# Kernel tuning notes

Measured on AMD Instinct MI355X. Metric: run time of the kernel, lower is better.

The kernel has to match this reference:

```python
import jax, jax.numpy as jnp
import numpy as np

T = 524288
D = 256
N = 8192

def setup_inputs() -> dict:
    key = jax.random.key(0)
    k1, k2, k3 = jax.random.split(key, 3)
    embedding = jax.random.normal(k1, (T, D), dtype=jnp.float32)
    W = jax.random.normal(k2, (D, D), dtype=jnp.float32) * (1.0 / np.sqrt(D))
    obj_to_img = jnp.sort(jax.random.randint(k3, (T,), 0, N))
    return {"embedding": embedding, "W": W, "obj_to_img": obj_to_img, "num_segments": N}

def reference(embedding, W, obj_to_img, num_segments):
    # Per-segment mean of embedding @ W  -> global context [N, D]
    proj = embedding @ W  # [T, D]
    seg_sum = jax.ops.segment_sum(proj, obj_to_img, num_segments=num_segments)  # [N, D]
    counts = jax.ops.segment_sum(jnp.ones((embedding.shape[0],), embedding.dtype),
                                 obj_to_img, num_segments=num_segments)  # [N]
    safe_counts = jnp.maximum(counts, 1.0)
    transformed_global = jnp.tanh(seg_sum / safe_counts[:, None])  # [N, D]
    # sigmoid(emb . tg[segment]) per token
    scores = jax.nn.sigmoid(jnp.sum(embedding * transformed_global[obj_to_img], axis=-1))  # [T]
    # per-segment weighted sum of embeddings
    rep = jax.ops.segment_sum(embedding * scores[:, None], obj_to_img, num_segments=num_segments)  # [N, D]
    # broadcast representation back to every token of its segment (repeat_interleave)
    return rep[obj_to_img]  # [T, D]
```

## Files before the change

kernel.cpp:

```cpp
#include <hip/hip_runtime.h>
#include <math.h>

#define D 256
#define NSEG 8192
#define SPB 16

__device__ __forceinline__ int lower_bound_dev(const int* __restrict__ a, int n, int key) {
    int lo = 0, hi = n;
    while (lo < hi) {
        int mid = (lo + hi) >> 1;
        if (a[mid] < key) lo = mid + 1; else hi = mid;
    }
    return lo;
}

__global__ void seg_sum_kernel(const float* __restrict__ emb,
                               const int* __restrict__ obj, int T,
                               float* __restrict__ S, int* __restrict__ counts) {
    const int seg   = blockIdx.x;
    const int start = lower_bound_dev(obj, T, seg);
    const int end   = lower_bound_dev(obj, T, seg + 1);
    const int tid  = threadIdx.x;
    const int lane = tid & 63;
    const int w    = tid >> 6;

    float4 acc = make_float4(0.f, 0.f, 0.f, 0.f);
    for (int r = start + w; r < end; r += 4) {
        const float4 e = *reinterpret_cast<const float4*>(emb + (size_t)r * D + lane * 4);
        acc.x += e.x; acc.y += e.y; acc.z += e.z; acc.w += e.w;
    }

    __shared__ float sm[4][D];
    *reinterpret_cast<float4*>(&sm[w][lane * 4]) = acc;
    __syncthreads();

    float v = sm[0][tid] + sm[1][tid] + sm[2][tid] + sm[3][tid];
    S[(size_t)seg * D + tid] = v;
    if (tid == 0) counts[seg] = end - start;
}

__global__ void proj_tanh_kernel(const float* __restrict__ S,
                                 const int* __restrict__ counts,
                                 const float* __restrict__ W,
                                 float* __restrict__ tg) {
    const int n0 = blockIdx.x * SPB;
    const int j  = threadIdx.x;

    __shared__ float Sl[SPB][D];
    __shared__ float inv[SPB];
    #pragma unroll
    for (int s = 0; s < SPB; ++s) Sl[s][j] = S[(size_t)(n0 + s) * D + j];
    if (j < SPB) {
        int c = counts[n0 + j];
        inv[j] = 1.0f / (float)(c > 1 ? c : 1);
    }
    __syncthreads();

    float acc[SPB];
    #pragma unroll
    for (int s = 0; s < SPB; ++s) acc[s] = 0.f;

    for (int k = 0; k < D; ++k) {
        const float wkj = W[k * D + j];
        #pragma unroll
        for (int s = 0; s < SPB; ++s) acc[s] += Sl[s][k] * wkj;
    }

    #pragma unroll
    for (int s = 0; s < SPB; ++s)
        tg[(size_t)(n0 + s) * D + j] = tanhf(acc[s] * inv[s]);
}

__global__ void score_rep_kernel(const float* __restrict__ emb,
                                 const int* __restrict__ obj, int T,
                                 const float* __restrict__ tg,
                                 float* __restrict__ out) {
    const int seg   = blockIdx.x;
    const int start = lower_bound_dev(obj, T, seg);
    const int end   = lower_bound_dev(obj, T, seg + 1);
    if (start >= end) return;

    const int tid  = threadIdx.x;
    const int lane = tid & 63;
    const int w    = tid >> 6;

    __shared__ float tgs[D];
    tgs[tid] = tg[(size_t)seg * D + tid];
    __syncthreads();
    const float4 tg4 = *reinterpret_cast<const float4*>(&tgs[lane * 4]);

    float4 acc = make_float4(0.f, 0.f, 0.f, 0.f);
    for (int r = start + w; r < end; r += 4) {
        const float4 e = *reinterpret_cast<const float4*>(emb + (size_t)r * D + lane * 4);
        float p = e.x * tg4.x + e.y * tg4.y + e.z * tg4.z + e.w * tg4.w;
        #pragma unroll
        for (int off = 32; off >= 1; off >>= 1) p += __shfl_xor(p, off, 64);
        const float score = 1.0f / (1.0f + __expf(-p));
        acc.x += e.x * score; acc.y += e.y * score;
        acc.z += e.z * score; acc.w += e.w * score;
    }

    __shared__ float rm[4][D];
    *reinterpret_cast<float4*>(&rm[w][lane * 4]) = acc;
    __syncthreads();
    rm[0][tid] = rm[0][tid] + rm[1][tid] + rm[2][tid] + rm[3][tid];
    __syncthreads();

    const float4 rep4 = *reinterpret_cast<const float4*>(&rm[0][lane * 4]);
    for (int r = start + w; r < end; r += 4) {
        *reinterpret_cast<float4*>(out + (size_t)r * D + lane * 4) = rep4;
    }
}

extern "C" void kernel_launch(void* const* d_in, const int* in_sizes, int n_in,
                              void* d_out, int out_size, void* d_ws, size_t ws_size,
                              hipStream_t stream) {
    const float* emb = (const float*)d_in[0];
    const float* W   = (const float*)d_in[1];
    const int*   obj = (const int*)d_in[2];
    const int T = in_sizes[2];

    float* out = (float*)d_out;

    float* S      = (float*)d_ws;
    float* tg     = S + (size_t)NSEG * D;
    int*   counts = (int*)(tg + (size_t)NSEG * D);

    seg_sum_kernel<<<NSEG, 256, 0, stream>>>(emb, obj, T, S, counts);
    proj_tanh_kernel<<<NSEG / SPB, 256, 0, stream>>>(S, counts, W, tg);
    score_rep_kernel<<<NSEG, 256, 0, stream>>>(emb, obj, T, tg, out);
}
```

Measured before the change: 1.019 ms.

## Fuse segment sum, projection, and scoring into one per-segment kernel

Replaces the three-kernel pipeline with a single kernel where each block sums its segment, computes the W projection and tanh for that segment, then performs the scoring and broadcast. This removes the intermediate S/tg global buffers and two launches, and lets the second pass over the segment's rows likely hit cache. In exchange, every block now streams the full W matrix with no cross-segment reuse, so W traffic rises sharply.

```diff
diff --git a/kernel.cpp b/kernel.cpp
--- a/kernel.cpp
+++ b/kernel.cpp
@@ -3,7 +3,6 @@
 
 #define D 256
 #define NSEG 8192
-#define SPB 16
 
 __device__ __forceinline__ int lower_bound_dev(const int* __restrict__ a, int n, int key) {
     int lo = 0, hi = n;
@@ -14,67 +13,11 @@
     return lo;
 }
 
-__global__ void seg_sum_kernel(const float* __restrict__ emb,
-                               const int* __restrict__ obj, int T,
-                               float* __restrict__ S, int* __restrict__ counts) {
-    const int seg   = blockIdx.x;
-    const int start = lower_bound_dev(obj, T, seg);
-    const int end   = lower_bound_dev(obj, T, seg + 1);
-    const int tid  = threadIdx.x;
-    const int lane = tid & 63;
-    const int w    = tid >> 6;
-
-    float4 acc = make_float4(0.f, 0.f, 0.f, 0.f);
-    for (int r = start + w; r < end; r += 4) {
-        const float4 e = *reinterpret_cast<const float4*>(emb + (size_t)r * D + lane * 4);
-        acc.x += e.x; acc.y += e.y; acc.z += e.z; acc.w += e.w;
-    }
-
-    __shared__ float sm[4][D];
-    *reinterpret_cast<float4*>(&sm[w][lane * 4]) = acc;
-    __syncthreads();
-
-    float v = sm[0][tid] + sm[1][tid] + sm[2][tid] + sm[3][tid];
-    S[(size_t)seg * D + tid] = v;
-    if (tid == 0) counts[seg] = end - start;
-}
-
-__global__ void proj_tanh_kernel(const float* __restrict__ S,
-                                 const int* __restrict__ counts,
-                                 const float* __restrict__ W,
-                                 float* __restrict__ tg) {
-    const int n0 = blockIdx.x * SPB;
-    const int j  = threadIdx.x;
-
-    __shared__ float Sl[SPB][D];
-    __shared__ float inv[SPB];
-    #pragma unroll
-    for (int s = 0; s < SPB; ++s) Sl[s][j] = S[(size_t)(n0 + s) * D + j];
-    if (j < SPB) {
-        int c = counts[n0 + j];
-        inv[j] = 1.0f / (float)(c > 1 ? c : 1);
-    }
-    __syncthreads();
-
-    float acc[SPB];
-    #pragma unroll
-    for (int s = 0; s < SPB; ++s) acc[s] = 0.f;
-
-    for (int k = 0; k < D; ++k) {
-        const float wkj = W[k * D + j];
-        #pragma unroll
-        for (int s = 0; s < SPB; ++s) acc[s] += Sl[s][k] * wkj;
-    }
-
-    #pragma unroll
-    for (int s = 0; s < SPB; ++s)
-        tg[(size_t)(n0 + s) * D + j] = tanhf(acc[s] * inv[s]);
-}
-
-__global__ void score_rep_kernel(const float* __restrict__ emb,
-                                 const int* __restrict__ obj, int T,
-                                 const float* __restrict__ tg,
-                                 float* __restrict__ out) {
+__global__ __launch_bounds__(256) void fused_seg_kernel(
+        const float* __restrict__ emb,
+        const float* __restrict__ W,
+        const int*   __restrict__ obj, int T,
+        float* __restrict__ out) {
     const int seg   = blockIdx.x;
     const int start = lower_bound_dev(obj, T, seg);
     const int end   = lower_bound_dev(obj, T, seg + 1);
@@ -84,29 +27,46 @@
     const int lane = tid & 63;
     const int w    = tid >> 6;
 
-    __shared__ float tgs[D];
-    tgs[tid] = tg[(size_t)seg * D + tid];
-    __syncthreads();
-    const float4 tg4 = *reinterpret_cast<const float4*>(&tgs[lane * 4]);
+    __shared__ float sm[4][D];
+    __shared__ float sv[D];
+    __shared__ float tg[D];
 
     float4 acc = make_float4(0.f, 0.f, 0.f, 0.f);
     for (int r = start + w; r < end; r += 4) {
         const float4 e = *reinterpret_cast<const float4*>(emb + (size_t)r * D + lane * 4);
-        float p = e.x * tg4.x + e.y * tg4.y + e.z * tg4.z + e.w * tg4.w;
-        #pragma unroll
-        for (int off = 32; off >= 1; off >>= 1) p += __shfl_xor(p, off, 64);
-        const float score = 1.0f / (1.0f + __expf(-p));
-        acc.x += e.x * score; acc.y += e.y * score;
-        acc.z += e.z * score; acc.w += e.w * score;
+        acc.x += e.x; acc.y += e.y; acc.z += e.z; acc.w += e.w;
     }
-
-    __shared__ float rm[4][D];
-    *reinterpret_cast<float4*>(&rm[w][lane * 4]) = acc;
+    *reinterpret_cast<float4*>(&sm[w][lane * 4]) = acc;
     __syncthreads();
-    rm[0][tid] = rm[0][tid] + rm[1][tid] + rm[2][tid] + rm[3][tid];
+    sv[tid] = sm[0][tid] + sm[1][tid] + sm[2][tid] + sm[3][tid];
     __syncthreads();
 
-    const float4 rep4 = *reinterpret_cast<const float4*>(&rm[0][lane * 4]);
+    const float inv = 1.0f / (float)(end - start);
+    float p = 0.f;
+    #pragma unroll 8
+    for (int k = 0; k < D; ++k) {
+        p += sv[k] * W[k * D + tid];
+    }
+    tg[tid] = tanhf(p * inv);
+    __syncthreads();
+    const float4 tg4 = *reinterpret_cast<const float4*>(&tg[lane * 4]);
+
+    float4 racc = make_float4(0.f, 0.f, 0.f, 0.f);
+    for (int r = start + w; r < end; r += 4) {
+        const float4 e = *reinterpret_cast<const float4*>(emb + (size_t)r * D + lane * 4);
+        float pd = e.x * tg4.x + e.y * tg4.y + e.z * tg4.z + e.w * tg4.w;
+        #pragma unroll
+        for (int off = 32; off >= 1; off >>= 1) pd += __shfl_xor(pd, off, 64);
+        const float score = 1.0f / (1.0f + __expf(-pd));
+        racc.x += e.x * score; racc.y += e.y * score;
+        racc.z += e.z * score; racc.w += e.w * score;
+    }
+    *reinterpret_cast<float4*>(&sm[w][lane * 4]) = racc;
+    __syncthreads();
+    sm[0][tid] = sm[0][tid] + sm[1][tid] + sm[2][tid] + sm[3][tid];
+    __syncthreads();
+    const float4 rep4 = *reinterpret_cast<const float4*>(&sm[0][lane * 4]);
+
     for (int r = start + w; r < end; r += 4) {
         *reinterpret_cast<float4*>(out + (size_t)r * D + lane * 4) = rep4;
     }
@@ -119,14 +79,7 @@
     const float* W   = (const float*)d_in[1];
     const int*   obj = (const int*)d_in[2];
     const int T = in_sizes[2];
-
     float* out = (float*)d_out;
 
-    float* S      = (float*)d_ws;
-    float* tg     = S + (size_t)NSEG * D;
-    int*   counts = (int*)(tg + (size_t)NSEG * D);
-
-    seg_sum_kernel<<<NSEG, 256, 0, stream>>>(emb, obj, T, S, counts);
-    proj_tanh_kernel<<<NSEG / SPB, 256, 0, stream>>>(S, counts, W, tg);
-    score_rep_kernel<<<NSEG, 256, 0, stream>>>(emb, obj, T, tg, out);
+    fused_seg_kernel<<<NSEG, 256, 0, stream>>>(emb, W, obj, T, out);
 }
```

Measured after the change: 991.0 us. 1.03x faster.
